# Performance work log

Hardware: AMD Instinct MI355X
Metric: run time of the kernel (lower is better)

Reference implementation:

```python
import jax, jax.numpy as jnp
import numpy as np

HID = 512
IN = 256
B = 64
T = 1024
ALPHA0 = 10.0 / 100.0  # dt / tau


def setup_inputs() -> dict:
    key = jax.random.key(0)
    k1, k2, k3, k4, k5 = jax.random.split(key, 5)
    x = jax.random.normal(k1, (B, T, IN), dtype=jnp.float32)
    init_state = jnp.zeros((B, HID), dtype=jnp.float32)
    W_in = jax.random.normal(k2, (IN, HID), dtype=jnp.float32) / np.sqrt(IN)
    b_in = jnp.zeros((HID,), dtype=jnp.float32)
    W_hid = jax.random.normal(k3, (HID, HID), dtype=jnp.float32) / np.sqrt(HID)
    b_hid = jnp.zeros((HID,), dtype=jnp.float32)
    alpha = jnp.full((HID,), ALPHA0, dtype=jnp.float32)
    return {"x": x, "init_state": init_state, "W_in": W_in, "b_in": b_in,
            "W_hid": W_hid, "b_hid": b_hid, "alpha": alpha}


def reference(x, init_state, W_in, b_in, W_hid, b_hid, alpha):
    # Precompute input projection for all timesteps (same math, batched GEMM)
    v_in = jnp.einsum('bti,ih->bth', x, W_in) + b_in  # (B, T, HID)

    def step(carry, v_in_t):
        fr_t, v_t = carry
        v_hid_t = fr_t @ W_hid + b_hid            # (B, HID)
        v_t = (1.0 - alpha) * v_t + alpha * (v_hid_t + v_in_t)
        fr_t = jax.nn.relu(v_t)
        return (fr_t, v_t), fr_t

    v0 = init_state
    fr0 = jax.nn.relu(v0)
    # scan over time axis
    _, frs = jax.lax.scan(step, (fr0, v0), jnp.swapaxes(v_in, 0, 1))
    return jnp.swapaxes(frs, 0, 1)  # (B, T, HID)
```

## Files before the change

kernel.cpp:

```cpp
#include <hip/hip_runtime.h>

#define HID 512
#define TSTEPS 1024

typedef short bf16x8 __attribute__((ext_vector_type(8)));
typedef float fx4 __attribute__((ext_vector_type(4)));
typedef unsigned ux2 __attribute__((ext_vector_type(2)));

__device__ __forceinline__ short f2bf(float f) {
  unsigned u = __builtin_bit_cast(unsigned, f);
  u = (u + 0x7fffu + ((u >> 16) & 1u)) >> 16;
  return (short)u;
}

__global__ __launch_bounds__(256) void vin_gemm(
    const float* __restrict__ x, const float* __restrict__ W_in,
    const float* __restrict__ b_in, const float* __restrict__ b_hid,
    float* __restrict__ out)
{
  __shared__ __align__(16) char smA[128 * 32 * 2];
  __shared__ __align__(16) char smB[128 * 32 * 2];
  const int tid = threadIdx.x;
  const int wave = tid >> 6, lane = tid & 63;
  const int lg = lane >> 4, lr = lane & 15;
  const int wm = wave >> 1, wn = wave & 1;
  const int r0 = blockIdx.x * 128, c0 = blockIdx.y * 128;

  fx4 acc[4][4] = {};

  const int arow = tid >> 3, aseg = tid & 7;
  const int bk = tid >> 3, bq = tid & 7;

  for (int k0 = 0; k0 < 256; k0 += 32) {
    #pragma unroll
    for (int q = 0; q < 4; ++q) {
      int row = arow + q * 32;
      fx4 fv = *(const fx4*)(x + (size_t)(r0 + row) * 256 + k0 + aseg * 4);
      ux2 p;
      p[0] = (unsigned)(unsigned short)f2bf(fv[0]) | ((unsigned)(unsigned short)f2bf(fv[1]) << 16);
      p[1] = (unsigned)(unsigned short)f2bf(fv[2]) | ((unsigned)(unsigned short)f2bf(fv[3]) << 16);
      int addr = (row * 64 + aseg * 8) ^ ((row & 7) << 4);
      *(ux2*)(smA + addr) = p;
    }
    #pragma unroll
    for (int q = 0; q < 4; ++q) {
      fx4 fv = *(const fx4*)(W_in + (size_t)(k0 + bk) * HID + c0 + q * 32 + bq * 4);
      #pragma unroll
      for (int e = 0; e < 4; ++e) {
        int col = q * 32 + bq * 4 + e;
        int addr = (col * 64 + bk * 2) ^ ((col & 7) << 4);
        *(short*)(smB + addr) = f2bf(fv[e]);
      }
    }
    __syncthreads();
    bf16x8 af[4];
    #pragma unroll
    for (int mt = 0; mt < 4; ++mt) {
      int row = wm * 64 + mt * 16 + lr;
      af[mt] = *(const bf16x8*)(smA + ((row * 64 + lg * 16) ^ ((row & 7) << 4)));
    }
    #pragma unroll
    for (int nt = 0; nt < 4; ++nt) {
      int col = wn * 64 + nt * 16 + lr;
      bf16x8 bf = *(const bf16x8*)(smB + ((col * 64 + lg * 16) ^ ((col & 7) << 4)));
      #pragma unroll
      for (int mt = 0; mt < 4; ++mt)
        acc[mt][nt] = __builtin_amdgcn_mfma_f32_16x16x32_bf16(af[mt], bf, acc[mt][nt], 0, 0, 0);
    }
    __syncthreads();
  }
  float bi[4];
  #pragma unroll
  for (int nt = 0; nt < 4; ++nt) {
    int c = c0 + wn * 64 + nt * 16 + lr;
    bi[nt] = b_in[c] + b_hid[c];
  }
  #pragma unroll
  for (int mt = 0; mt < 4; ++mt)
    #pragma unroll
    for (int nt = 0; nt < 4; ++nt)
      #pragma unroll
      for (int jj = 0; jj < 4; ++jj) {
        int grow = r0 + wm * 64 + mt * 16 + lg * 4 + jj;
        int gcol = c0 + wn * 64 + nt * 16 + lr;
        out[(size_t)grow * HID + gcol] = acc[mt][nt][jj] + bi[nt];
      }
}

__global__ __launch_bounds__(512) void pack_w(const float* __restrict__ W_hid,
                                              short* __restrict__ ws)
{
  const int tid = threadIdx.x;
  const int wave = tid >> 6, lane = tid & 63;
  const int lg = lane >> 4, lr = lane & 15;
  const int col = wave * 64 + 32 + lr;
  for (int kk = 0; kk < 16; ++kk) {
    bf16x8 w;
    #pragma unroll
    for (int j = 0; j < 8; ++j)
      w[j] = f2bf(W_hid[(size_t)(kk * 32 + lg * 8 + j) * HID + col]);
    *(bf16x8*)(ws + ((size_t)((wave * 16 + kk) * 64 + lane)) * 8) = w;
  }
}

#define FR0_OFF (128 * 1024)

__global__ __launch_bounds__(512, 2) void rnn_scan(
    float* base,
    const float* __restrict__ init_state,
    const float* __restrict__ W_hid,
    const float* __restrict__ alpha,
    const short* __restrict__ wsf)
{
  extern __shared__ __align__(16) char smem[];
  const int tid = threadIdx.x;
  const int wave = tid >> 6, lane = tid & 63;
  const int lg = lane >> 4, lr = lane & 15;
  const int bwg = blockIdx.x;
  const int cb = wave * 64;

  bf16x8 wreg[2][16];
  #pragma unroll
  for (int nt = 0; nt < 4; ++nt) {
    if (nt == 2) continue;
    const int col = cb + nt * 16 + lr;
    #pragma unroll
    for (int kk = 0; kk < 16; ++kk) {
      const int k0 = kk * 32 + lg * 8;
      bf16x8 w;
      #pragma unroll
      for (int j = 0; j < 8; ++j)
        w[j] = f2bf(W_hid[(size_t)(k0 + j) * HID + col]);
      if (nt < 2) {
        wreg[nt][kk] = w;
      } else {
        const int cw = wave * 16 + lr;
        int addr = (cw * 1024 + kk * 64 + lg * 16) ^ ((cw & 7) << 4);
        *(bf16x8*)(smem + addr) = w;
      }
    }
  }

  float al[4], v[4][4];
  #pragma unroll
  for (int nt = 0; nt < 4; ++nt) al[nt] = alpha[cb + nt * 16 + lr];
  #pragma unroll
  for (int nt = 0; nt < 4; ++nt)
    #pragma unroll
    for (int jj = 0; jj < 4; ++jj)
      v[nt][jj] = init_state[(size_t)(bwg * 16 + lg * 4 + jj) * HID + cb + nt * 16 + lr];

  #pragma unroll
  for (int nt = 0; nt < 4; ++nt)
    #pragma unroll
    for (int jj = 0; jj < 4; ++jj) {
      int row = lg * 4 + jj;
      int addr = (FR0_OFF + row * 1024 + (cb + nt * 16 + lr) * 2) ^ (lg << 5);
      *(short*)(smem + addr) = f2bf(fmaxf(v[nt][jj], 0.f));
    }

  int off[4];
  #pragma unroll
  for (int jj = 0; jj < 4; ++jj)
    off[jj] = (lg * 4 + jj) * TSTEPS * HID + cb + lr;
  float* bb = base + (size_t)bwg * 16 * TSTEPS * HID;

  fx4 acc[4];
  #pragma unroll
  for (int nt = 0; nt < 4; ++nt)
    #pragma unroll
    for (int jj = 0; jj < 4; ++jj)
      acc[nt][jj] = bb[off[jj] + nt * 16];

  const bf16x8* wsp = (const bf16x8*)(wsf + ((size_t)(wave * 16) * 64 + lane) * 8);
  bf16x8 wst[16];
  wst[0] = wsp[0];   wst[1] = wsp[64];  wst[2] = wsp[128]; wst[3] = wsp[192];

  __syncthreads();

  const int aswz = (lr >> 2) << 5;
  const int abase0 = lr * 1024 + lg * 16;
  const int cw = wave * 16 + lr;
  const int wbase = cw * 1024 + lg * 16;
  const int wswz = (cw & 7) << 4;
  const int frwswz = lg << 5;

  for (int t = 0; t < TSTEPS; ++t) {
    const int rb = FR0_OFF + ((t & 1) << 14);
    const int wb = FR0_OFF + (((t + 1) & 1) << 14);

    #pragma unroll
    for (int kk = 0; kk < 16; ++kk) {
      if (kk == 0) {
        wst[4] = wsp[4 * 64];  wst[5] = wsp[5 * 64];
        wst[6] = wsp[6 * 64];  wst[7] = wsp[7 * 64];
      }
      if (kk == 4) {
        wst[8]  = wsp[8 * 64];  wst[9]  = wsp[9 * 64];
        wst[10] = wsp[10 * 64]; wst[11] = wsp[11 * 64];
      }
      if (kk == 8) {
        wst[12] = wsp[12 * 64]; wst[13] = wsp[13 * 64];
        wst[14] = wsp[14 * 64]; wst[15] = wsp[15 * 64];
      }
      bf16x8 a  = *(const bf16x8*)(smem + ((rb + abase0 + kk * 64) ^ aswz));
      bf16x8 b3 = *(const bf16x8*)(smem + ((wbase + kk * 64) ^ wswz));
      acc[0] = __builtin_amdgcn_mfma_f32_16x16x32_bf16(a, wreg[0][kk], acc[0], 0, 0, 0);
      acc[1] = __builtin_amdgcn_mfma_f32_16x16x32_bf16(a, wreg[1][kk], acc[1], 0, 0, 0);
      acc[2] = __builtin_amdgcn_mfma_f32_16x16x32_bf16(a, wst[kk],     acc[2], 0, 0, 0);
      acc[3] = __builtin_amdgcn_mfma_f32_16x16x32_bf16(a, b3,          acc[3], 0, 0, 0);
    }

    #pragma unroll
    for (int nt = 0; nt < 4; ++nt)
      #pragma unroll
      for (int jj = 0; jj < 4; ++jj) {
        float nv = v[nt][jj] + al[nt] * (acc[nt][jj] - v[nt][jj]);
        v[nt][jj] = nv;
        float fr = fmaxf(nv, 0.f);
        bb[t * HID + off[jj] + nt * 16] = fr;
        int row = lg * 4 + jj;
        int addr = (wb + row * 1024 + (cb + nt * 16 + lr) * 2) ^ frwswz;
        *(short*)(smem + addr) = f2bf(fr);
      }

    if (t + 1 < TSTEPS) {
      #pragma unroll
      for (int nt = 0; nt < 4; ++nt)
        #pragma unroll
        for (int jj = 0; jj < 4; ++jj)
          acc[nt][jj] = bb[(t + 1) * HID + off[jj] + nt * 16];
    }
    wst[0] = wsp[0];   wst[1] = wsp[64];  wst[2] = wsp[128]; wst[3] = wsp[192];

    __syncthreads();
  }
}

extern "C" void kernel_launch(void* const* d_in, const int* in_sizes, int n_in,
                              void* d_out, int out_size, void* d_ws, size_t ws_size,
                              hipStream_t stream) {
  const float* x     = (const float*)d_in[0];
  const float* inist = (const float*)d_in[1];
  const float* W_in  = (const float*)d_in[2];
  const float* b_in  = (const float*)d_in[3];
  const float* W_hid = (const float*)d_in[4];
  const float* b_hid = (const float*)d_in[5];
  const float* alph  = (const float*)d_in[6];
  float* out = (float*)d_out;
  (void)in_sizes; (void)n_in; (void)out_size; (void)ws_size;

  pack_w<<<dim3(1), dim3(512), 0, stream>>>(W_hid, (short*)d_ws);
  vin_gemm<<<dim3(512, 4), dim3(256), 0, stream>>>(x, W_in, b_in, b_hid, out);

  (void)hipFuncSetAttribute(reinterpret_cast<const void*>(rnn_scan),
                            hipFuncAttributeMaxDynamicSharedMemorySize, 160 * 1024);
  rnn_scan<<<dim3(4), dim3(512), 160 * 1024, stream>>>(out, inist, W_hid, alph,
                                                       (const short*)d_ws);
}
```

Baseline: 4.078 ms.

## Transpose RNN scan MFMA so each lane owns contiguous hidden columns

The recurrent MFMA is reorganised with weights as the A operand and firing rates as B, so each lane holds four consecutive hidden units for one batch row. Global loads and stores of v_in and outputs become 16-byte vector accesses, and the LDS layouts for the firing-rate buffers and the LDS-resident weight slice become unswizzled, lane-contiguous 16-byte accesses. The streamed weight registers shrink to an 8-entry ring refilled inside the k-loop, and the next step's v_in prefetch is spread across the loop. Alpha is stored as packed bf16 to save registers, which lowers its precision.

```diff
diff --git a/kernel.cpp b/kernel.cpp
--- a/kernel.cpp
+++ b/kernel.cpp
@@ -27,7 +27,6 @@
   const int r0 = blockIdx.x * 128, c0 = blockIdx.y * 128;
 
   fx4 acc[4][4] = {};
-
   const int arow = tid >> 3, aseg = tid & 7;
   const int bk = tid >> 3, bq = tid & 7;
 
@@ -121,8 +120,7 @@
 
   bf16x8 wreg[2][16];
   #pragma unroll
-  for (int nt = 0; nt < 4; ++nt) {
-    if (nt == 2) continue;
+  for (int nt = 0; nt < 2; ++nt) {
     const int col = cb + nt * 16 + lr;
     #pragma unroll
     for (int kk = 0; kk < 16; ++kk) {
@@ -131,107 +129,112 @@
       #pragma unroll
       for (int j = 0; j < 8; ++j)
         w[j] = f2bf(W_hid[(size_t)(k0 + j) * HID + col]);
-      if (nt < 2) {
-        wreg[nt][kk] = w;
-      } else {
-        const int cw = wave * 16 + lr;
-        int addr = (cw * 1024 + kk * 64 + lg * 16) ^ ((cw & 7) << 4);
-        *(bf16x8*)(smem + addr) = w;
-      }
-    }
-  }
-
-  float al[4], v[4][4];
-  #pragma unroll
-  for (int nt = 0; nt < 4; ++nt) al[nt] = alpha[cb + nt * 16 + lr];
+      wreg[nt][kk] = w;
+    }
+  }
+  {
+    const int col = cb + 48 + lr;
+    for (int kk = 0; kk < 16; ++kk) {
+      bf16x8 w;
+      #pragma unroll
+      for (int j = 0; j < 8; ++j)
+        w[j] = f2bf(W_hid[(size_t)(kk * 32 + lg * 8 + j) * HID + col]);
+      *(bf16x8*)(smem + wave * 16384 + kk * 1024 + lane * 16) = w;
+    }
+  }
+
+  int hoff[4];
+  #pragma unroll
+  for (int nt = 0; nt < 4; ++nt) hoff[nt] = cb + nt * 16 + lg * 4;
+
+  unsigned al2[8];
+  #pragma unroll
+  for (int nt = 0; nt < 4; ++nt) {
+    fx4 a4 = *(const fx4*)(alpha + hoff[nt]);
+    al2[nt * 2]     = (unsigned)(unsigned short)f2bf(a4[0]) | ((unsigned)(unsigned short)f2bf(a4[1]) << 16);
+    al2[nt * 2 + 1] = (unsigned)(unsigned short)f2bf(a4[2]) | ((unsigned)(unsigned short)f2bf(a4[3]) << 16);
+  }
+
+  float v[4][4];
+  #pragma unroll
+  for (int nt = 0; nt < 4; ++nt) {
+    fx4 iv = *(const fx4*)(init_state + (size_t)(bwg * 16 + lr) * HID + hoff[nt]);
+    #pragma unroll
+    for (int j = 0; j < 4; ++j) v[nt][j] = iv[j];
+  }
+
+  int fw[4];
   #pragma unroll
   for (int nt = 0; nt < 4; ++nt)
-    #pragma unroll
-    for (int jj = 0; jj < 4; ++jj)
-      v[nt][jj] = init_state[(size_t)(bwg * 16 + lg * 4 + jj) * HID + cb + nt * 16 + lr];
-
-  #pragma unroll
-  for (int nt = 0; nt < 4; ++nt)
-    #pragma unroll
-    for (int jj = 0; jj < 4; ++jj) {
-      int row = lg * 4 + jj;
-      int addr = (FR0_OFF + row * 1024 + (cb + nt * 16 + lr) * 2) ^ (lg << 5);
-      *(short*)(smem + addr) = f2bf(fmaxf(v[nt][jj], 0.f));
-    }
-
-  int off[4];
-  #pragma unroll
-  for (int jj = 0; jj < 4; ++jj)
-    off[jj] = (lg * 4 + jj) * TSTEPS * HID + cb + lr;
-  float* bb = base + (size_t)bwg * 16 * TSTEPS * HID;
-
-  fx4 acc[4];
-  #pragma unroll
-  for (int nt = 0; nt < 4; ++nt)
-    #pragma unroll
-    for (int jj = 0; jj < 4; ++jj)
-      acc[nt][jj] = bb[off[jj] + nt * 16];
-
-  const bf16x8* wsp = (const bf16x8*)(wsf + ((size_t)(wave * 16) * 64 + lane) * 8);
-  bf16x8 wst[16];
-  wst[0] = wsp[0];   wst[1] = wsp[64];  wst[2] = wsp[128]; wst[3] = wsp[192];
+    fw[nt] = (wave * 2 + (nt >> 1)) * 1024 + ((((nt & 1) * 2 + (lg >> 1)) * 16 + lr) * 16) + ((lg & 1) * 8);
+
+  #pragma unroll
+  for (int nt = 0; nt < 4; ++nt) {
+    ux2 pw;
+    pw[0] = (unsigned)(unsigned short)f2bf(fmaxf(v[nt][0], 0.f)) |
+            ((unsigned)(unsigned short)f2bf(fmaxf(v[nt][1], 0.f)) << 16);
+    pw[1] = (unsigned)(unsigned short)f2bf(fmaxf(v[nt][2], 0.f)) |
+            ((unsigned)(unsigned short)f2bf(fmaxf(v[nt][3], 0.f)) << 16);
+    *(ux2*)(smem + FR0_OFF + fw[nt]) = pw;
+  }
+
+  float* bb = base + (size_t)(bwg * 16 + lr) * TSTEPS * HID;
+
+  fx4 vld[4];
+  #pragma unroll
+  for (int nt = 0; nt < 4; ++nt) vld[nt] = *(const fx4*)(bb + hoff[nt]);
+
+  const bf16x8* wsp = (const bf16x8*)wsf + ((size_t)wave * 16 * 64 + lane);
+  bf16x8 wst[8];
+  #pragma unroll
+  for (int s = 0; s < 8; ++s) wst[s] = wsp[s * 64];
 
   __syncthreads();
 
-  const int aswz = (lr >> 2) << 5;
-  const int abase0 = lr * 1024 + lg * 16;
-  const int cw = wave * 16 + lr;
-  const int wbase = cw * 1024 + lg * 16;
-  const int wswz = (cw & 7) << 4;
-  const int frwswz = lg << 5;
+  const int wldsbase = wave * 16384 + lane * 16;
+  const int frrd = lane * 16;
 
   for (int t = 0; t < TSTEPS; ++t) {
     const int rb = FR0_OFF + ((t & 1) << 14);
-    const int wb = FR0_OFF + (((t + 1) & 1) << 14);
+    const int wbuf = FR0_OFF + (((t + 1) & 1) << 14);
+    const int tn = (t + 1 < TSTEPS) ? t + 1 : t;
+
+    fx4 acc[4];
+    #pragma unroll
+    for (int nt = 0; nt < 4; ++nt) acc[nt] = vld[nt];
 
     #pragma unroll
     for (int kk = 0; kk < 16; ++kk) {
-      if (kk == 0) {
-        wst[4] = wsp[4 * 64];  wst[5] = wsp[5 * 64];
-        wst[6] = wsp[6 * 64];  wst[7] = wsp[7 * 64];
+      bf16x8 fb = *(const bf16x8*)(smem + rb + kk * 1024 + frrd);
+      bf16x8 w3 = *(const bf16x8*)(smem + wldsbase + kk * 1024);
+      acc[0] = __builtin_amdgcn_mfma_f32_16x16x32_bf16(wreg[0][kk], fb, acc[0], 0, 0, 0);
+      acc[1] = __builtin_amdgcn_mfma_f32_16x16x32_bf16(wreg[1][kk], fb, acc[1], 0, 0, 0);
+      acc[2] = __builtin_amdgcn_mfma_f32_16x16x32_bf16(wst[kk & 7], fb, acc[2], 0, 0, 0);
+      acc[3] = __builtin_amdgcn_mfma_f32_16x16x32_bf16(w3, fb, acc[3], 0, 0, 0);
+      if (kk < 8)  wst[kk] = wsp[(kk + 8) * 64];
+      if (kk >= 4 && kk < 8) vld[kk - 4] = *(const fx4*)(bb + (size_t)tn * HID + hoff[kk - 4]);
+      if (kk >= 9) wst[kk - 9] = wsp[(kk - 9) * 64];
+    }
+
+    #pragma unroll
+    for (int nt = 0; nt < 4; ++nt) {
+      fx4 st;
+      #pragma unroll
+      for (int j = 0; j < 4; ++j) {
+        unsigned u = al2[nt * 2 + (j >> 1)];
+        float aj = __builtin_bit_cast(float, (j & 1) ? (u & 0xffff0000u) : (u << 16));
+        float nv = v[nt][j] + aj * (acc[nt][j] - v[nt][j]);
+        v[nt][j] = nv;
+        st[j] = fmaxf(nv, 0.f);
       }
-      if (kk == 4) {
-        wst[8]  = wsp[8 * 64];  wst[9]  = wsp[9 * 64];
-        wst[10] = wsp[10 * 64]; wst[11] = wsp[11 * 64];
-      }
-      if (kk == 8) {
-        wst[12] = wsp[12 * 64]; wst[13] = wsp[13 * 64];
-        wst[14] = wsp[14 * 64]; wst[15] = wsp[15 * 64];
-      }
-      bf16x8 a  = *(const bf16x8*)(smem + ((rb + abase0 + kk * 64) ^ aswz));
-      bf16x8 b3 = *(const bf16x8*)(smem + ((wbase + kk * 64) ^ wswz));
-      acc[0] = __builtin_amdgcn_mfma_f32_16x16x32_bf16(a, wreg[0][kk], acc[0], 0, 0, 0);
-      acc[1] = __builtin_amdgcn_mfma_f32_16x16x32_bf16(a, wreg[1][kk], acc[1], 0, 0, 0);
-      acc[2] = __builtin_amdgcn_mfma_f32_16x16x32_bf16(a, wst[kk],     acc[2], 0, 0, 0);
-      acc[3] = __builtin_amdgcn_mfma_f32_16x16x32_bf16(a, b3,          acc[3], 0, 0, 0);
-    }
-
-    #pragma unroll
-    for (int nt = 0; nt < 4; ++nt)
-      #pragma unroll
-      for (int jj = 0; jj < 4; ++jj) {
-        float nv = v[nt][jj] + al[nt] * (acc[nt][jj] - v[nt][jj]);
-        v[nt][jj] = nv;
-        float fr = fmaxf(nv, 0.f);
-        bb[t * HID + off[jj] + nt * 16] = fr;
-        int row = lg * 4 + jj;
-        int addr = (wb + row * 1024 + (cb + nt * 16 + lr) * 2) ^ frwswz;
-        *(short*)(smem + addr) = f2bf(fr);
-      }
-
-    if (t + 1 < TSTEPS) {
-      #pragma unroll
-      for (int nt = 0; nt < 4; ++nt)
-        #pragma unroll
-        for (int jj = 0; jj < 4; ++jj)
-          acc[nt][jj] = bb[(t + 1) * HID + off[jj] + nt * 16];
-    }
-    wst[0] = wsp[0];   wst[1] = wsp[64];  wst[2] = wsp[128]; wst[3] = wsp[192];
+      *(fx4*)(bb + (size_t)t * HID + hoff[nt]) = st;
+      ux2 pw;
+      pw[0] = (unsigned)(unsigned short)f2bf(st[0]) | ((unsigned)(unsigned short)f2bf(st[1]) << 16);
+      pw[1] = (unsigned)(unsigned short)f2bf(st[2]) | ((unsigned)(unsigned short)f2bf(st[3]) << 16);
+      *(ux2*)(smem + wbuf + fw[nt]) = pw;
+    }
+
+    wst[7] = wsp[7 * 64];
 
     __syncthreads();
   }
```

Result: slower. 4.633 ms (+13.6%).
